# Optimization experiments

Measured on AMD Instinct MI355X. Metric: run time of the kernel, lower is better.

## Reference

```python
import jax, jax.numpy as jnp
import numpy as np

N_VOXELS = 262144  # active output voxels (stride=1 -> same coord set as input)


def setup_inputs() -> dict:
    key = jax.random.key(0)
    k1, k2, k3, k4 = jax.random.split(key, 4)
    N, C_IN, C_OUT, K, M = N_VOXELS, 64, 64, 27, 65536
    x = jax.random.normal(k1, (N, C_IN), dtype=jnp.float32)
    W = jax.random.normal(k2, (K, C_IN, C_OUT), dtype=jnp.float32) * (1.0 / np.sqrt(C_IN * K))
    in_map = jax.random.randint(k3, (K, M), 0, N, dtype=jnp.int32)
    out_map = jax.random.randint(k4, (K, M), 0, N, dtype=jnp.int32)
    return {"x": x, "W": W, "in_map": in_map, "out_map": out_map}


def reference(x, W, in_map, out_map):
    # Sparse (Minkowski-style) convolution: gather -> per-offset GEMM -> scatter-add.
    # x: [N, Cin], W: [K, Cin, Cout], in_map/out_map: [K, M] indices into voxel list.
    N = x.shape[0]
    C_out = W.shape[-1]
    gathered = x[in_map]                              # [K, M, Cin]  (irregular gather)
    msg = jnp.einsum('kmc,kcd->kmd', gathered, W)     # [K, M, Cout] per-offset GEMM
    out = jnp.zeros((N, C_out), dtype=x.dtype)
    out = out.at[out_map.reshape(-1)].add(msg.reshape(-1, C_out))  # scatter-add
    return out
```

## Files before the change

kernel.cpp:

```cpp
#include <hip/hip_runtime.h>


typedef __attribute__((ext_vector_type(8))) short bf16x8;
typedef __attribute__((ext_vector_type(8))) unsigned short u16x8;
typedef __attribute__((ext_vector_type(4))) unsigned short u16x4;
typedef __attribute__((ext_vector_type(4))) float f32x4;
typedef __attribute__((ext_vector_type(2))) float f32x2;

constexpr int KOFF = 27;
constexpr int M = 65536;
constexpr int CIN = 64;
constexpr int COUT = 64;
constexpr int NVOX = 262144;
constexpr int NMSG = KOFF * M;
constexpr int TM_BLOCK = 512;
constexpr int TILES_PER_K = M / TM_BLOCK;
constexpr int SUBTILES = TM_BLOCK / (4 * 16);
constexpr int XCVT_BLOCKS = NVOX * CIN / 8 / 256;
constexpr int ZERO_BLOCKS = NVOX / (256 * 4);

static __device__ __forceinline__ short f2bf(float f) {
  unsigned u = __builtin_bit_cast(unsigned, f);
  unsigned r = (u + 0x7FFFu + ((u >> 16) & 1u)) >> 16;
  return (short)r;
}
static __device__ __forceinline__ float bf2f(unsigned short h) {
  return __builtin_bit_cast(float, (unsigned)h << 16);
}


__global__ __launch_bounds__(256) void xw_kernel(
    const float* __restrict__ x, const float* __restrict__ W,
    unsigned short* __restrict__ xb, unsigned short* __restrict__ Wf,
    int* __restrict__ starts, int xcvtBlocks) {
  const int b = blockIdx.x;
  if (b < xcvtBlocks) {
    int i = b * 256 + threadIdx.x;
    const float4* p = (const float4*)x + (size_t)i * 2;
    float4 a = p[0], q = p[1];
    u16x8 h;
    h[0] = (unsigned short)f2bf(a.x); h[1] = (unsigned short)f2bf(a.y);
    h[2] = (unsigned short)f2bf(a.z); h[3] = (unsigned short)f2bf(a.w);
    h[4] = (unsigned short)f2bf(q.x); h[5] = (unsigned short)f2bf(q.y);
    h[6] = (unsigned short)f2bf(q.z); h[7] = (unsigned short)f2bf(q.w);
    *(u16x8*)(xb + (size_t)i * 8) = h;
  } else if (b < xcvtBlocks + KOFF) {
    int k = b - xcvtBlocks;
    const float* Wk = W + (size_t)k * (CIN * COUT);
    unsigned short* dst = Wf + (size_t)k * 4096;
#pragma unroll
    for (int i = 0; i < 16; ++i) {
      int e = threadIdx.x * 16 + i;
      int j = e & 7, l = (e >> 3) & 63, tu = e >> 9;
      int t = tu >> 1, u = tu & 1;
      dst[e] = (unsigned short)f2bf(Wk[(u * 32 + (l >> 4) * 8 + j) * COUT + t * 16 + (l & 15)]);
    }
  } else {
    int zb = b - xcvtBlocks - KOFF;
    int i = (zb * 256 + threadIdx.x) * 4;
    *(int4*)(starts + i) = make_int4(0, 0, 0, 0);
  }
}


__global__ __launch_bounds__(256) void rank_kernel(const int* __restrict__ out_map,
                                                   int* __restrict__ starts,
                                                   int* __restrict__ rank) {
  int i = (blockIdx.x * 256 + threadIdx.x) * 4;
  int4 om = *(const int4*)(out_map + i);
  int4 rk;
  rk.x = atomicAdd(&starts[om.x], 1);
  rk.y = atomicAdd(&starts[om.y], 1);
  rk.z = atomicAdd(&starts[om.z], 1);
  rk.w = atomicAdd(&starts[om.w], 1);
  *(int4*)(rank + i) = rk;
}


__global__ __launch_bounds__(256) void scan1_kernel(int* __restrict__ starts,
                                                    int* __restrict__ blockSums) {
  __shared__ int s[256];
  int t = threadIdx.x, i = blockIdx.x * 256 + t;
  int c = starts[i];
  s[t] = c; __syncthreads();
  for (int off = 1; off < 256; off <<= 1) {
    int add = (t >= off) ? s[t - off] : 0;
    __syncthreads(); s[t] += add; __syncthreads();
  }
  starts[i] = s[t] - c;
  if (t == 255) blockSums[blockIdx.x] = s[t];
}

__global__ __launch_bounds__(256) void scan2_kernel(int* __restrict__ bs) {
  __shared__ int s[256];
  int t = threadIdx.x;
  int v0 = bs[t*4], v1 = bs[t*4+1], v2 = bs[t*4+2], v3 = bs[t*4+3];
  int sum = v0 + v1 + v2 + v3;
  s[t] = sum; __syncthreads();
  for (int off = 1; off < 256; off <<= 1) {
    int add = (t >= off) ? s[t - off] : 0;
    __syncthreads(); s[t] += add; __syncthreads();
  }
  int run = s[t] - sum;
  bs[t*4] = run; run += v0;
  bs[t*4+1] = run; run += v1;
  bs[t*4+2] = run; run += v2;
  bs[t*4+3] = run;
}

__global__ __launch_bounds__(256) void scan3_kernel(int* __restrict__ starts,
                                                    const int* __restrict__ blockBase) {
  int i = blockIdx.x * 256 + threadIdx.x;
  starts[i] += blockBase[blockIdx.x];
  if (i == 0) starts[NVOX] = NMSG;
}


template <bool BF16IN>
__global__ __launch_bounds__(256) void gemm_msg_kernel(
    const void* __restrict__ xin, const unsigned short* __restrict__ Wf,
    const int* __restrict__ in_map, const int* __restrict__ out_map,
    const int* __restrict__ rank, const int* __restrict__ starts,
    unsigned short* __restrict__ msg) {
  const int k = blockIdx.x / TILES_PER_K;
  const int mblock = (blockIdx.x % TILES_PER_K) * TM_BLOCK;
  const int wave = threadIdx.x >> 6;
  const int l = threadIdx.x & 63;
  const int lg = l >> 4;
  const int lr = l & 15;

  bf16x8 bfrag[4][2];
  const bf16x8* wf = (const bf16x8*)(Wf + (size_t)k * 4096);
#pragma unroll
  for (int t = 0; t < 4; ++t)
#pragma unroll
    for (int u = 0; u < 2; ++u)
      bfrag[t][u] = wf[(t * 2 + u) * 64 + l];

  const int mwave = mblock + wave * (TM_BLOCK / 4);
  const int rb = k * M + mwave;

  auto loadA = [&](int s, bf16x8& A0, bf16x8& A1) {
    int id = in_map[rb + s * 16 + lr];
    if (BF16IN) {
      const unsigned short* xr = (const unsigned short*)xin + (size_t)id * CIN + lg * 8;
      A0 = *(const bf16x8*)(xr);
      A1 = *(const bf16x8*)(xr + 32);
    } else {
      const float* xr = (const float*)xin + (size_t)id * CIN + lg * 8;
      float4 x0 = *(const float4*)(xr);
      float4 x1 = *(const float4*)(xr + 4);
      float4 x2 = *(const float4*)(xr + 32);
      float4 x3 = *(const float4*)(xr + 36);
      A0[0]=f2bf(x0.x); A0[1]=f2bf(x0.y); A0[2]=f2bf(x0.z); A0[3]=f2bf(x0.w);
      A0[4]=f2bf(x1.x); A0[5]=f2bf(x1.y); A0[6]=f2bf(x1.z); A0[7]=f2bf(x1.w);
      A1[0]=f2bf(x2.x); A1[1]=f2bf(x2.y); A1[2]=f2bf(x2.z); A1[3]=f2bf(x2.w);
      A1[4]=f2bf(x3.x); A1[5]=f2bf(x3.y); A1[6]=f2bf(x3.z); A1[7]=f2bf(x3.w);
    }
  };

  int om[4], rk[4];
#pragma unroll
  for (int r = 0; r < 4; ++r) {
    om[r] = out_map[rb + lg * 4 + r];
    rk[r] = rank[rb + lg * 4 + r];
  }

  bf16x8 c0, c1, n0, n1;
  loadA(0, c0, c1);
  loadA(1, n0, n1);

#pragma unroll 1
  for (int s = 0; s < SUBTILES; ++s) {
    bf16x8 p0, p1;
    const bool have = (s + 2 < SUBTILES);
    if (have) loadA(s + 2, p0, p1);

    int omN[4], rkN[4];
    if (s + 1 < SUBTILES) {
      const int rowb = rb + (s + 1) * 16 + lg * 4;
#pragma unroll
      for (int r = 0; r < 4; ++r) { omN[r] = out_map[rowb + r]; rkN[r] = rank[rowb + r]; }
    } else {
#pragma unroll
      for (int r = 0; r < 4; ++r) { omN[r] = 0; rkN[r] = 0; }
    }
    int st[4];
#pragma unroll
    for (int r = 0; r < 4; ++r) st[r] = starts[om[r]];

    f32x4 acc[4] = {{0.f,0.f,0.f,0.f},{0.f,0.f,0.f,0.f},{0.f,0.f,0.f,0.f},{0.f,0.f,0.f,0.f}};
#pragma unroll
    for (int t = 0; t < 4; ++t) {
      acc[t] = __builtin_amdgcn_mfma_f32_16x16x32_bf16(c0, bfrag[t][0], acc[t], 0, 0, 0);
      acc[t] = __builtin_amdgcn_mfma_f32_16x16x32_bf16(c1, bfrag[t][1], acc[t], 0, 0, 0);
    }

#pragma unroll
    for (int r = 0; r < 4; ++r) {
      const int sl = st[r] + rk[r];
      u16x4 h;
      h[0] = (unsigned short)f2bf(acc[0][r]);
      h[1] = (unsigned short)f2bf(acc[1][r]);
      h[2] = (unsigned short)f2bf(acc[2][r]);
      h[3] = (unsigned short)f2bf(acc[3][r]);
      __builtin_nontemporal_store(h, (u16x4*)(msg + (size_t)sl * 64 + lr * 4));
    }

    c0 = n0; c1 = n1;
    if (have) { n0 = p0; n1 = p1; }
#pragma unroll
    for (int r = 0; r < 4; ++r) { om[r] = omN[r]; rk[r] = rkN[r]; }
  }
}


__global__ __launch_bounds__(256) void gather_out_kernel(
    const unsigned short* __restrict__ msg, const int* __restrict__ starts,
    float* __restrict__ out) {
  const int wid = (blockIdx.x * 256 + threadIdx.x) >> 6;
  const int p = threadIdx.x & 63;
  const int r = p >> 3;
  const int c = p & 7;
  const int o = wid * 8 + r;

  const int base = starts[o];
  const int n = starts[o + 1] - base;
  const unsigned short* src = msg + (size_t)base * 64 + c * 8;

  u16x8 v[8];
#pragma unroll
  for (int i = 0; i < 8; ++i) {
    int safe = (i < n) ? i : 0;
    v[i] = __builtin_nontemporal_load((const u16x8*)(src + (size_t)safe * 64));
  }
  float acc[8] = {};
#pragma unroll
  for (int i = 0; i < 8; ++i) {
    float m = (i < n) ? 1.0f : 0.0f;
#pragma unroll
    for (int d = 0; d < 8; ++d)
      acc[d] = fmaf(m, bf2f((unsigned short)v[i][d]), acc[d]);
  }
  for (int i = 8; i < n; ++i) {
    u16x8 t = __builtin_nontemporal_load((const u16x8*)(src + (size_t)i * 64));
#pragma unroll
    for (int d = 0; d < 8; ++d) acc[d] += bf2f((unsigned short)t[d]);
  }

  float* orow = out + (size_t)o * 64 + 2 * c;
  f32x2 s0 = {acc[0], acc[4]};
  f32x2 s1 = {acc[1], acc[5]};
  f32x2 s2 = {acc[2], acc[6]};
  f32x2 s3 = {acc[3], acc[7]};
  __builtin_nontemporal_store(s0, (f32x2*)(orow));
  __builtin_nontemporal_store(s1, (f32x2*)(orow + 16));
  __builtin_nontemporal_store(s2, (f32x2*)(orow + 32));
  __builtin_nontemporal_store(s3, (f32x2*)(orow + 48));
}


__global__ __launch_bounds__(256) void spconv_atomic_kernel(
    const float* __restrict__ x, const float* __restrict__ W,
    const int* __restrict__ in_map, const int* __restrict__ out_map,
    float* __restrict__ out) {
  const int k = blockIdx.x / TILES_PER_K;
  const int mblock = (blockIdx.x % TILES_PER_K) * TM_BLOCK;
  const int wave = threadIdx.x >> 6;
  const int l = threadIdx.x & 63;
  const int lg = l >> 4;
  const int lr = l & 15;
  bf16x8 bfrag[4][2];
  const float* Wk = W + (size_t)k * (CIN * COUT);
#pragma unroll
  for (int t = 0; t < 4; ++t)
#pragma unroll
    for (int u = 0; u < 2; ++u)
#pragma unroll
      for (int j = 0; j < 8; ++j)
        bfrag[t][u][j] = f2bf(Wk[(u * 32 + lg * 8 + j) * COUT + t * 16 + lr]);
  const int mwave = mblock + wave * (TM_BLOCK / 4);
#pragma unroll 1
  for (int s = 0; s < SUBTILES; ++s) {
    const int mbase = mwave + s * 16;
    const int in_idx = in_map[k * M + mbase + lr];
    const float* xr = x + (size_t)in_idx * CIN + lg * 8;
    float4 x0 = *(const float4*)(xr);
    float4 x1 = *(const float4*)(xr + 4);
    float4 x2 = *(const float4*)(xr + 32);
    float4 x3 = *(const float4*)(xr + 36);
    bf16x8 a0, a1;
    a0[0]=f2bf(x0.x); a0[1]=f2bf(x0.y); a0[2]=f2bf(x0.z); a0[3]=f2bf(x0.w);
    a0[4]=f2bf(x1.x); a0[5]=f2bf(x1.y); a0[6]=f2bf(x1.z); a0[7]=f2bf(x1.w);
    a1[0]=f2bf(x2.x); a1[1]=f2bf(x2.y); a1[2]=f2bf(x2.z); a1[3]=f2bf(x2.w);
    a1[4]=f2bf(x3.x); a1[5]=f2bf(x3.y); a1[6]=f2bf(x3.z); a1[7]=f2bf(x3.w);
    f32x4 acc[4] = {{0.f,0.f,0.f,0.f},{0.f,0.f,0.f,0.f},{0.f,0.f,0.f,0.f},{0.f,0.f,0.f,0.f}};
#pragma unroll
    for (int t = 0; t < 4; ++t) {
      acc[t] = __builtin_amdgcn_mfma_f32_16x16x32_bf16(a0, bfrag[t][0], acc[t], 0, 0, 0);
      acc[t] = __builtin_amdgcn_mfma_f32_16x16x32_bf16(a1, bfrag[t][1], acc[t], 0, 0, 0);
    }
    const int obase = k * M + mbase + lg * 4;
    int oidx[4];
#pragma unroll
    for (int r = 0; r < 4; ++r) oidx[r] = out_map[obase + r];
#pragma unroll
    for (int t = 0; t < 4; ++t)
#pragma unroll
      for (int r = 0; r < 4; ++r)
        atomicAdd(out + (size_t)oidx[r] * COUT + t * 16 + lr, acc[t][r]);
  }
}

extern "C" void kernel_launch(void* const* d_in, const int* in_sizes, int n_in,
                              void* d_out, int out_size, void* d_ws, size_t ws_size,
                              hipStream_t stream) {
  const float* x = (const float*)d_in[0];
  const float* W = (const float*)d_in[1];
  const int* in_map = (const int*)d_in[2];
  const int* out_map = (const int*)d_in[3];
  float* out = (float*)d_out;
  char* ws = (char*)d_ws;

  const size_t msg_b    = (size_t)NMSG * 128;
  const size_t xb_b     = (size_t)NVOX * CIN * 2;
  const size_t rank_b   = (size_t)NMSG * 4;
  const size_t wf_b     = (size_t)KOFF * 4096 * 2;
  const size_t starts_b = (size_t)(NVOX + 1) * 4;
  const size_t bsum_b   = 1024 * 4;
  auto pad = [](size_t b) { return (b + 255) & ~(size_t)255; };

  size_t need_p1 = pad(msg_b) + pad(rank_b) + pad(wf_b) + pad(starts_b) + pad(bsum_b);
  size_t need_p0 = need_p1 + pad(xb_b);
  bool useXb = (ws_size >= need_p0);

  if (ws_size < need_p1) {
    hipMemsetAsync(d_out, 0, (size_t)out_size * sizeof(float), stream);
    spconv_atomic_kernel<<<dim3(KOFF * TILES_PER_K), dim3(256), 0, stream>>>(
        x, W, in_map, out_map, out);
    return;
  }

  size_t off = 0;
  unsigned short* msg = (unsigned short*)(ws + off); off += pad(msg_b);
  unsigned short* xb = nullptr;
  if (useXb) { xb = (unsigned short*)(ws + off); off += pad(xb_b); }
  int* rank = (int*)(ws + off); off += pad(rank_b);
  unsigned short* Wf = (unsigned short*)(ws + off); off += pad(wf_b);
  int* starts = (int*)(ws + off); off += pad(starts_b);
  int* bsum = (int*)(ws + off);

  int xcvtBlocks = useXb ? XCVT_BLOCKS : 0;
  xw_kernel<<<dim3(xcvtBlocks + KOFF + ZERO_BLOCKS), dim3(256), 0, stream>>>(
      x, W, xb, Wf, starts, xcvtBlocks);

  rank_kernel<<<dim3(NMSG / 1024), dim3(256), 0, stream>>>(out_map, starts, rank);

  scan1_kernel<<<dim3(NVOX / 256), dim3(256), 0, stream>>>(starts, bsum);
  scan2_kernel<<<dim3(1), dim3(256), 0, stream>>>(bsum);
  scan3_kernel<<<dim3(NVOX / 256), dim3(256), 0, stream>>>(starts, bsum);

  if (useXb)
    gemm_msg_kernel<true><<<dim3(KOFF * TILES_PER_K), dim3(256), 0, stream>>>(
        (const void*)xb, Wf, in_map, out_map, rank, starts, msg);
  else
    gemm_msg_kernel<false><<<dim3(KOFF * TILES_PER_K), dim3(256), 0, stream>>>(
        (const void*)x, Wf, in_map, out_map, rank, starts, msg);

  gather_out_kernel<<<dim3(NVOX / 32), dim3(256), 0, stream>>>(msg, starts, out);
}
```

Measured before the change: 223.2 us.

## Split offsets into groups so message buffer stays cache-resident

New measurement: 270.9 us. 1.21x slower.

```diff
diff --git a/kernel.cpp b/kernel.cpp
--- a/kernel.cpp
+++ b/kernel.cpp
@@ -13,11 +13,15 @@
 constexpr int COUT = 64;
 constexpr int NVOX = 262144;
 constexpr int NMSG = KOFF * M;
+constexpr int G = 3;
+constexpr int KG = KOFF / G;
+constexpr int MPG = KG * M;
 constexpr int TM_BLOCK = 512;
 constexpr int TILES_PER_K = M / TM_BLOCK;
 constexpr int SUBTILES = TM_BLOCK / (4 * 16);
 constexpr int XCVT_BLOCKS = NVOX * CIN / 8 / 256;
-constexpr int ZERO_BLOCKS = NVOX / (256 * 4);
+constexpr int ZERO_BLOCKS = G * NVOX / (256 * 4);
+constexpr int RANK_BPG = MPG / 1024;
 
 static __device__ __forceinline__ short f2bf(float f) {
   unsigned u = __builtin_bit_cast(unsigned, f);
@@ -66,13 +70,15 @@
 __global__ __launch_bounds__(256) void rank_kernel(const int* __restrict__ out_map,
                                                    int* __restrict__ starts,
                                                    int* __restrict__ rank) {
+  int g = blockIdx.x / RANK_BPG;
+  int* cnt = starts + (size_t)g * NVOX;
   int i = (blockIdx.x * 256 + threadIdx.x) * 4;
   int4 om = *(const int4*)(out_map + i);
   int4 rk;
-  rk.x = atomicAdd(&starts[om.x], 1);
-  rk.y = atomicAdd(&starts[om.y], 1);
-  rk.z = atomicAdd(&starts[om.z], 1);
-  rk.w = atomicAdd(&starts[om.w], 1);
+  rk.x = atomicAdd(&cnt[om.x], 1);
+  rk.y = atomicAdd(&cnt[om.y], 1);
+  rk.z = atomicAdd(&cnt[om.z], 1);
+  rk.w = atomicAdd(&cnt[om.w], 1);
   *(int4*)(rank + i) = rk;
 }
 
@@ -93,8 +99,9 @@
 
 __global__ __launch_bounds__(256) void scan2_kernel(int* __restrict__ bs) {
   __shared__ int s[256];
+  int base = blockIdx.x * 1024;
   int t = threadIdx.x;
-  int v0 = bs[t*4], v1 = bs[t*4+1], v2 = bs[t*4+2], v3 = bs[t*4+3];
+  int v0 = bs[base+t*4], v1 = bs[base+t*4+1], v2 = bs[base+t*4+2], v3 = bs[base+t*4+3];
   int sum = v0 + v1 + v2 + v3;
   s[t] = sum; __syncthreads();
   for (int off = 1; off < 256; off <<= 1) {
@@ -102,17 +109,16 @@
     __syncthreads(); s[t] += add; __syncthreads();
   }
   int run = s[t] - sum;
-  bs[t*4] = run; run += v0;
-  bs[t*4+1] = run; run += v1;
-  bs[t*4+2] = run; run += v2;
-  bs[t*4+3] = run;
+  bs[base+t*4] = run; run += v0;
+  bs[base+t*4+1] = run; run += v1;
+  bs[base+t*4+2] = run; run += v2;
+  bs[base+t*4+3] = run;
 }
 
 __global__ __launch_bounds__(256) void scan3_kernel(int* __restrict__ starts,
                                                     const int* __restrict__ blockBase) {
   int i = blockIdx.x * 256 + threadIdx.x;
   starts[i] += blockBase[blockIdx.x];
-  if (i == 0) starts[NVOX] = NMSG;
 }
 
 
@@ -120,9 +126,9 @@
 __global__ __launch_bounds__(256) void gemm_msg_kernel(
     const void* __restrict__ xin, const unsigned short* __restrict__ Wf,
     const int* __restrict__ in_map, const int* __restrict__ out_map,
-    const int* __restrict__ rank, const int* __restrict__ starts,
-    unsigned short* __restrict__ msg) {
-  const int k = blockIdx.x / TILES_PER_K;
+    const int* __restrict__ rank, const int* __restrict__ gstarts,
+    unsigned short* __restrict__ msg, int g) {
+  const int k = g * KG + blockIdx.x / TILES_PER_K;
   const int mblock = (blockIdx.x % TILES_PER_K) * TM_BLOCK;
   const int wave = threadIdx.x >> 6;
   const int l = threadIdx.x & 63;
@@ -187,7 +193,7 @@
     }
     int st[4];
 #pragma unroll
-    for (int r = 0; r < 4; ++r) st[r] = starts[om[r]];
+    for (int r = 0; r < 4; ++r) st[r] = gstarts[om[r]];
 
     f32x4 acc[4] = {{0.f,0.f,0.f,0.f},{0.f,0.f,0.f,0.f},{0.f,0.f,0.f,0.f},{0.f,0.f,0.f,0.f}};
 #pragma unroll
@@ -204,7 +210,7 @@
       h[1] = (unsigned short)f2bf(acc[1][r]);
       h[2] = (unsigned short)f2bf(acc[2][r]);
       h[3] = (unsigned short)f2bf(acc[3][r]);
-      __builtin_nontemporal_store(h, (u16x4*)(msg + (size_t)sl * 64 + lr * 4));
+      *(u16x4*)(msg + (size_t)sl * 64 + lr * 4) = h;
     }
 
     c0 = n0; c1 = n1;
@@ -215,8 +221,9 @@
 }
 
 
+template <bool ACCUM>
 __global__ __launch_bounds__(256) void gather_out_kernel(
-    const unsigned short* __restrict__ msg, const int* __restrict__ starts,
+    const unsigned short* __restrict__ msg, const int* __restrict__ gstarts,
     float* __restrict__ out) {
   const int wid = (blockIdx.x * 256 + threadIdx.x) >> 6;
   const int p = threadIdx.x & 63;
@@ -224,15 +231,16 @@
   const int c = p & 7;
   const int o = wid * 8 + r;
 
-  const int base = starts[o];
-  const int n = starts[o + 1] - base;
+  const int base = gstarts[o];
+  const int nxt = (o == NVOX - 1) ? MPG : gstarts[o + 1];
+  const int n = nxt - base;
   const unsigned short* src = msg + (size_t)base * 64 + c * 8;
 
   u16x8 v[8];
 #pragma unroll
   for (int i = 0; i < 8; ++i) {
     int safe = (i < n) ? i : 0;
-    v[i] = __builtin_nontemporal_load((const u16x8*)(src + (size_t)safe * 64));
+    v[i] = *(const u16x8*)(src + (size_t)safe * 64);
   }
   float acc[8] = {};
 #pragma unroll
@@ -243,7 +251,7 @@
       acc[d] = fmaf(m, bf2f((unsigned short)v[i][d]), acc[d]);
   }
   for (int i = 8; i < n; ++i) {
-    u16x8 t = __builtin_nontemporal_load((const u16x8*)(src + (size_t)i * 64));
+    u16x8 t = *(const u16x8*)(src + (size_t)i * 64);
 #pragma unroll
     for (int d = 0; d < 8; ++d) acc[d] += bf2f((unsigned short)t[d]);
   }
@@ -253,10 +261,16 @@
   f32x2 s1 = {acc[1], acc[5]};
   f32x2 s2 = {acc[2], acc[6]};
   f32x2 s3 = {acc[3], acc[7]};
-  __builtin_nontemporal_store(s0, (f32x2*)(orow));
-  __builtin_nontemporal_store(s1, (f32x2*)(orow + 16));
-  __builtin_nontemporal_store(s2, (f32x2*)(orow + 32));
-  __builtin_nontemporal_store(s3, (f32x2*)(orow + 48));
+  if (ACCUM) {
+    f32x2 q0 = *(f32x2*)(orow);      s0 += q0;
+    f32x2 q1 = *(f32x2*)(orow + 16); s1 += q1;
+    f32x2 q2 = *(f32x2*)(orow + 32); s2 += q2;
+    f32x2 q3 = *(f32x2*)(orow + 48); s3 += q3;
+  }
+  *(f32x2*)(orow)      = s0;
+  *(f32x2*)(orow + 16) = s1;
+  *(f32x2*)(orow + 32) = s2;
+  *(f32x2*)(orow + 48) = s3;
 }
 
 
@@ -322,12 +336,12 @@
   float* out = (float*)d_out;
   char* ws = (char*)d_ws;
 
-  const size_t msg_b    = (size_t)NMSG * 128;
+  const size_t msg_b    = (size_t)MPG * 128;
   const size_t xb_b     = (size_t)NVOX * CIN * 2;
   const size_t rank_b   = (size_t)NMSG * 4;
   const size_t wf_b     = (size_t)KOFF * 4096 * 2;
-  const size_t starts_b = (size_t)(NVOX + 1) * 4;
-  const size_t bsum_b   = 1024 * 4;
+  const size_t starts_b = (size_t)G * NVOX * 4;
+  const size_t bsum_b   = (size_t)G * 1024 * 4;
   auto pad = [](size_t b) { return (b + 255) & ~(size_t)255; };
 
   size_t need_p1 = pad(msg_b) + pad(rank_b) + pad(wf_b) + pad(starts_b) + pad(bsum_b);
@@ -356,16 +370,21 @@
 
   rank_kernel<<<dim3(NMSG / 1024), dim3(256), 0, stream>>>(out_map, starts, rank);
 
-  scan1_kernel<<<dim3(NVOX / 256), dim3(256), 0, stream>>>(starts, bsum);
-  scan2_kernel<<<dim3(1), dim3(256), 0, stream>>>(bsum);
-  scan3_kernel<<<dim3(NVOX / 256), dim3(256), 0, stream>>>(starts, bsum);
-
-  if (useXb)
-    gemm_msg_kernel<true><<<dim3(KOFF * TILES_PER_K), dim3(256), 0, stream>>>(
-        (const void*)xb, Wf, in_map, out_map, rank, starts, msg);
-  else
-    gemm_msg_kernel<false><<<dim3(KOFF * TILES_PER_K), dim3(256), 0, stream>>>(
-        (const void*)x, Wf, in_map, out_map, rank, starts, msg);
-
-  gather_out_kernel<<<dim3(NVOX / 32), dim3(256), 0, stream>>>(msg, starts, out);
-}
+  scan1_kernel<<<dim3(G * 1024), dim3(256), 0, stream>>>(starts, bsum);
+  scan2_kernel<<<dim3(G), dim3(256), 0, stream>>>(bsum);
+  scan3_kernel<<<dim3(G * 1024), dim3(256), 0, stream>>>(starts, bsum);
+
+  for (int g = 0; g < G; ++g) {
+    const int* gst = starts + (size_t)g * NVOX;
+    if (useXb)
+      gemm_msg_kernel<true><<<dim3(KG * TILES_PER_K), dim3(256), 0, stream>>>(
+          (const void*)xb, Wf, in_map, out_map, rank, gst, msg, g);
+    else
+      gemm_msg_kernel<false><<<dim3(KG * TILES_PER_K), dim3(256), 0, stream>>>(
+          (const void*)x, Wf, in_map, out_map, rank, gst, msg, g);
+    if (g == 0)
+      gather_out_kernel<false><<<dim3(NVOX / 32), dim3(256), 0, stream>>>(msg, gst, out);
+    else
+      gather_out_kernel<true><<<dim3(NVOX / 32), dim3(256), 0, stream>>>(msg, gst, out);
+  }
+}
```
